# Performance work log

Measured on AMD Instinct MI355X. Metric: run time of the kernel, lower is better.

## Reference

```python
import jax, jax.numpy as jnp
import numpy as np

EPS = 1e-7  # K.epsilon()
ROUTINGS = 3

def squash(v, axis=-1):
    s2 = jnp.sum(jnp.square(v), axis=axis, keepdims=True)
    scale = s2 / (1.0 + s2)
    return scale * v / jnp.sqrt(s2 + EPS)

def setup_inputs() -> dict:
    key = jax.random.key(0)
    k1, k2 = jax.random.split(key)
    B, N, I, D, E = 16, 64, 2048, 32, 16
    x = jax.random.normal(k1, (B, I, E), dtype=jnp.float32)
    # glorot-uniform-ish scale for W [N, I, D, E]
    limit = np.sqrt(6.0 / (E + D)).astype(np.float32)
    W = jax.random.uniform(k2, (N, I, D, E), dtype=jnp.float32, minval=-limit, maxval=limit)
    return {"x": x, "W": W}

def reference(x, W):
    # x: [B, I, E]; W: [N, I, D, E]
    # u_hat[b,n,i,d] = sum_e W[n,i,d,e] * x[b,i,e]
    u_hat = jnp.einsum('nide,bie->bnid', W, x)  # [B, N, I, D]
    B, N, I, _ = u_hat.shape
    b = jnp.zeros((B, N, I), dtype=u_hat.dtype)
    outputs = None
    for i in range(ROUTINGS):
        c = jax.nn.softmax(b, axis=1)                     # softmax over num_capsule
        s = jnp.einsum('bni,bnid->bnd', c, u_hat)         # weighted sum
        outputs = squash(s)                               # [B, N, D]
        if i < ROUTINGS - 1:
            b = b + jnp.einsum('bnd,bnid->bni', outputs, u_hat)
    return outputs
```

## Files before the change

### kernel.cpp

```cpp
#include <hip/hip_runtime.h>
#include <cstdint>


#define B_ 16
#define N_ 64
#define I_ 2048
#define D_ 32
#define E_ 16
#define EPS_ 1e-7f
#define IPER_ 8
#define NCHUNK_ 256
#define GRIDP_ 512
#define SROW_ 2048
#define NOUT_ 32768
#define PSTRIDE_ 32768
#define WN4_ 262144

template <int CTRL>
__device__ __forceinline__ float dppf(float v) {
  return __int_as_float(
      __builtin_amdgcn_update_dpp(0, __float_as_int(v), CTRL, 0xF, 0xF, true));
}

__device__ __forceinline__ void chunk_u(const float4 wa0, const float4 wa1,
                                        const float* __restrict__ xr,
                                        int k, int q, float& u0, float& u1)
{
  float p0[4], p1[4];
#pragma unroll
  for (int j = 0; j < 4; ++j) {
    const float4 xv = *(const float4*)&xr[(4 * k + j) * E_ + 4 * q];
    p0[j] = wa0.x * xv.x + wa0.y * xv.y + wa0.z * xv.z + wa0.w * xv.w;
    p1[j] = wa1.x * xv.x + wa1.y * xv.y + wa1.z * xv.z + wa1.w * xv.w;
  }
  {
    const float r0 = p0[0] + dppf<0xB1>(p0[0]);
    const float r1 = p0[1] + dppf<0xB1>(p0[1]);
    const float r2 = p0[2] + dppf<0xB1>(p0[2]);
    const float r3 = p0[3] + dppf<0xB1>(p0[3]);
    const float sa = (q & 1) ? r1 : r0;
    const float sb = (q & 1) ? r3 : r2;
    const float a0 = sa + dppf<0x4E>(sa);
    const float a1 = sb + dppf<0x4E>(sb);
    u0 = (q & 2) ? a1 : a0;
  }
  {
    const float r0 = p1[0] + dppf<0xB1>(p1[0]);
    const float r1 = p1[1] + dppf<0xB1>(p1[1]);
    const float r2 = p1[2] + dppf<0xB1>(p1[2]);
    const float r3 = p1[3] + dppf<0xB1>(p1[3]);
    const float sa = (q & 1) ? r1 : r0;
    const float sb = (q & 1) ? r3 : r2;
    const float a0 = sa + dppf<0x4E>(sa);
    const float a1 = sb + dppf<0x4E>(sb);
    u1 = (q & 2) ? a1 : a0;
  }
}

template <int MODE>
__global__ __launch_bounds__(512)
__attribute__((amdgpu_waves_per_eu(4, 4)))
void caps_pass(
    const float* __restrict__ W,
    const float* __restrict__ x,
    const float* __restrict__ vtot,
    float* __restrict__ out,
    int use_part)
{
  const int t = threadIdx.x;
  const int w = t >> 6;
  const int l = t & 63;
  const int q = l & 3;
  const int dd = l >> 2;

  const int orig = blockIdx.x;
  const int h = (orig >> 3) & 1;
  const int ic = (orig & 7) | ((orig >> 4) << 3);
  const int i0 = ic * IPER_;

  __shared__ float x_lds[IPER_ * 8 * E_];
  __shared__ float2 u_st[16 * 512];
  __shared__ float l2[N_ * 33];
  __shared__ float c_lds[N_ * 9];

  for (int j = t; j < IPER_ * 8 * E_; j += 512) {
    const int ii = j >> 7, bl = (j >> 4) & 7, e = j & 15;
    x_lds[j] = x[((size_t)(h * 8 + bl) * I_ + (i0 + ii)) * E_ + e];
  }
  __syncthreads();

  float acc0[8][2], acc1[8][2];
#pragma unroll
  for (int nn = 0; nn < 8; ++nn)
#pragma unroll
    for (int k = 0; k < 2; ++k) { acc0[nn][k] = 0.f; acc1[nn][k] = 0.f; }

  float vt0[8][2], vt1[8][2];
  if (MODE == 1) {
#pragma unroll
    for (int nn = 0; nn < 8; ++nn)
#pragma unroll
      for (int k = 0; k < 2; ++k) {
        const size_t va = (size_t)(h * 8 + 4 * k + q) * SROW_ +
                          (size_t)(8 * w + nn) * D_ + dd;
        vt0[nn][k] = vtot[va];
        vt1[nn][k] = vtot[va + 16];
      }
  }

  const float4* Wbase = (const float4*)W + (((size_t)(8 * w) * I_ + i0) << 7);

#pragma unroll 1
  for (int ii = 0; ii < IPER_; ++ii) {
    const float* xr = &x_lds[ii * (8 * E_)];

#pragma unroll
    for (int g = 0; g < 4; ++g) {
      const float4* W0 = Wbase + (size_t)(2 * g) * WN4_ + ii * 128;
      const float4* W1 = W0 + WN4_;
      const float4 a0 = W0[l], a1 = W0[64 + l];
      const float4 b0 = W1[l], b1 = W1[64 + l];
#pragma unroll
      for (int s = 0; s < 2; ++s) {
        const int nn = 2 * g + s;
        const float4 wv0 = s ? b0 : a0;
        const float4 wv1 = s ? b1 : a1;
#pragma unroll
        for (int k = 0; k < 2; ++k) {
          float u0, u1;
          chunk_u(wv0, wv1, xr, k, q, u0, u1);
          if (MODE == 0) {
            acc0[nn][k] += u0;
            acc1[nn][k] += u1;
          } else {
            u_st[(nn * 2 + k) * 512 + t] = make_float2(u0, u1);
            float lp = vt0[nn][k] * u0 + vt1[nn][k] * u1;
            lp += dppf<0x124>(lp);
            lp += dppf<0x128>(lp);
            if ((l & 12) == 0)
              l2[(8 * w + nn) * 33 + (4 * k + q) * 4 + (l >> 4)] = lp;
          }
        }
      }
    }

    if (MODE == 1) {
      __syncthreads();
      {
        const int bw = t >> 6, j = t & 63;
        const int base = j * 33 + bw * 4;
        const float raw = l2[base] + l2[base + 1] + l2[base + 2] + l2[base + 3];
        float m = raw;
#pragma unroll
        for (int off = 32; off; off >>= 1) m = fmaxf(m, __shfl_xor(m, off));
        const float e = __expf(raw - m);
        float den = e;
#pragma unroll
        for (int off = 32; off; off >>= 1) den += __shfl_xor(den, off);
        c_lds[j * 9 + bw] = e / den;
      }
      __syncthreads();
#pragma unroll
      for (int nn = 0; nn < 8; ++nn)
#pragma unroll
        for (int k = 0; k < 2; ++k) {
          const float2 u = u_st[(nn * 2 + k) * 512 + t];
          const float cc = c_lds[(8 * w + nn) * 9 + 4 * k + q];
          acc0[nn][k] += cc * u.x;
          acc1[nn][k] += cc * u.y;
        }
    }
  }

  const float sc = (MODE == 0) ? (1.f / 64.f) : 1.f;
  float* base = out + (use_part ? (size_t)ic * PSTRIDE_ : 0);
#pragma unroll
  for (int nn = 0; nn < 8; ++nn) {
#pragma unroll
    for (int k = 0; k < 2; ++k) {
      const int b = h * 8 + 4 * k + q, n = 8 * w + nn;
      const size_t a = (size_t)b * SROW_ + (size_t)n * D_ + dd;
      if (use_part) {
        base[a] = acc0[nn][k] * sc;
        base[a + 16] = acc1[nn][k] * sc;
      } else {
        atomicAdd(&base[a], acc0[nn][k] * sc);
        atomicAdd(&base[a + 16], acc1[nn][k] * sc);
      }
    }
  }
}

template <int ACCMODE>
__global__ __launch_bounds__(256) void reduce_squash(
    const float* __restrict__ part, const float* __restrict__ s_single,
    float* __restrict__ dst, int use_part)
{
  const int g = blockIdx.x * 256 + threadIdx.x;
  float sum;
  if (use_part) {
    sum = 0.f;
#pragma unroll 8
    for (int p = 0; p < NCHUNK_; ++p) sum += part[(size_t)p * PSTRIDE_ + g];
  } else {
    sum = s_single[g];
  }
  float s2 = sum * sum;
#pragma unroll
  for (int off = 16; off; off >>= 1) s2 += __shfl_xor(s2, off);
  const float f = s2 / ((1.f + s2) * sqrtf(s2 + EPS_));
  if (ACCMODE == 0) dst[g] = sum * f;
  else dst[g] += sum * f;
}

extern "C" void kernel_launch(void* const* d_in, const int* in_sizes, int n_in,
                              void* d_out, int out_size, void* d_ws, size_t ws_size,
                              hipStream_t stream)
{
  const float* x = (const float*)d_in[0];
  const float* W = (const float*)d_in[1];
  float* s = (float*)d_out;
  float* vtot = (float*)d_ws;
  float* part = vtot + NOUT_;

  const size_t need =
      ((size_t)NOUT_ + (size_t)NCHUNK_ * PSTRIDE_) * sizeof(float);
  const int use_part = (ws_size >= need) ? 1 : 0;
  float* pass_out = use_part ? part : s;
  const size_t sbytes = (size_t)NOUT_ * sizeof(float);

  if (!use_part) hipMemsetAsync(s, 0, sbytes, stream);
  caps_pass<0><<<GRIDP_, 512, 0, stream>>>(W, x, vtot, pass_out, use_part);
  reduce_squash<0><<<128, 256, 0, stream>>>(part, s, vtot, use_part);

  if (!use_part) hipMemsetAsync(s, 0, sbytes, stream);
  caps_pass<1><<<GRIDP_, 512, 0, stream>>>(W, x, vtot, pass_out, use_part);
  reduce_squash<1><<<128, 256, 0, stream>>>(part, s, vtot, use_part);

  if (!use_part) hipMemsetAsync(s, 0, sbytes, stream);
  caps_pass<1><<<GRIDP_, 512, 0, stream>>>(W, x, vtot, pass_out, use_part);
  reduce_squash<0><<<128, 256, 0, stream>>>(part, s, s, use_part);
}
```

Before: 313.0 us.

## Split batch across four block groups to double grid and raise occupancy

Each block now handles 4 batch rows instead of 8, so the grid doubles to 1024 blocks. Per-thread accumulators, shared-memory buffers and the routing-softmax work shrink accordingly, and the waves-per-EU hint is relaxed to allow up to 8 waves. This targets latency hiding and occupancy in the pass kernels. The cost is that each W tile is now fetched by twice as many blocks, which increases global/L2 traffic for W, and half the threads sit idle during the softmax step.

```diff
diff --git a/kernel.cpp b/kernel.cpp
--- a/kernel.cpp
+++ b/kernel.cpp
@@ -7,10 +7,11 @@
 #define I_ 2048
 #define D_ 32
 #define E_ 16
+#define QB_ 4
 #define EPS_ 1e-7f
 #define IPER_ 8
 #define NCHUNK_ 256
-#define GRIDP_ 512
+#define GRIDP_ 1024
 #define SROW_ 2048
 #define NOUT_ 32768
 #define PSTRIDE_ 32768
@@ -22,14 +23,14 @@
       __builtin_amdgcn_update_dpp(0, __float_as_int(v), CTRL, 0xF, 0xF, true));
 }
 
-__device__ __forceinline__ void chunk_u(const float4 wa0, const float4 wa1,
-                                        const float* __restrict__ xr,
-                                        int k, int q, float& u0, float& u1)
+__device__ __forceinline__ void chunk4(const float4 wa0, const float4 wa1,
+                                       const float* __restrict__ xr,
+                                       int q, float& u0, float& u1)
 {
   float p0[4], p1[4];
 #pragma unroll
   for (int j = 0; j < 4; ++j) {
-    const float4 xv = *(const float4*)&xr[(4 * k + j) * E_ + 4 * q];
+    const float4 xv = *(const float4*)&xr[j * E_ + 4 * q];
     p0[j] = wa0.x * xv.x + wa0.y * xv.y + wa0.z * xv.z + wa0.w * xv.w;
     p1[j] = wa1.x * xv.x + wa1.y * xv.y + wa1.z * xv.z + wa1.w * xv.w;
   }
@@ -59,7 +60,7 @@
 
 template <int MODE>
 __global__ __launch_bounds__(512)
-__attribute__((amdgpu_waves_per_eu(4, 4)))
+__attribute__((amdgpu_waves_per_eu(8)))
 void caps_pass(
     const float* __restrict__ W,
     const float* __restrict__ x,
@@ -74,45 +75,41 @@
   const int dd = l >> 2;
 
   const int orig = blockIdx.x;
-  const int h = (orig >> 3) & 1;
-  const int ic = (orig & 7) | ((orig >> 4) << 3);
+  const int h = (orig >> 3) & 3;
+  const int ic = (orig & 7) | ((orig >> 5) << 3);
   const int i0 = ic * IPER_;
 
-  __shared__ float x_lds[IPER_ * 8 * E_];
-  __shared__ float2 u_st[16 * 512];
-  __shared__ float l2[N_ * 33];
-  __shared__ float c_lds[N_ * 9];
-
-  for (int j = t; j < IPER_ * 8 * E_; j += 512) {
-    const int ii = j >> 7, bl = (j >> 4) & 7, e = j & 15;
-    x_lds[j] = x[((size_t)(h * 8 + bl) * I_ + (i0 + ii)) * E_ + e];
+  __shared__ float x_lds[IPER_ * QB_ * E_];
+  __shared__ float2 u_st[(MODE == 1) ? 8 * 512 : 1];
+  __shared__ float l2[(MODE == 1) ? N_ * 17 : 1];
+  __shared__ float c_lds[(MODE == 1) ? N_ * 5 : 1];
+
+  {
+    const int ii = t >> 6, bl = (t >> 4) & 3, e = t & 15;
+    x_lds[t] = x[((size_t)(h * QB_ + bl) * I_ + (i0 + ii)) * E_ + e];
   }
   __syncthreads();
 
-  float acc0[8][2], acc1[8][2];
-#pragma unroll
-  for (int nn = 0; nn < 8; ++nn)
-#pragma unroll
-    for (int k = 0; k < 2; ++k) { acc0[nn][k] = 0.f; acc1[nn][k] = 0.f; }
-
-  float vt0[8][2], vt1[8][2];
+  float acc0[8], acc1[8];
+#pragma unroll
+  for (int nn = 0; nn < 8; ++nn) { acc0[nn] = 0.f; acc1[nn] = 0.f; }
+
+  float vt0[8], vt1[8];
   if (MODE == 1) {
 #pragma unroll
-    for (int nn = 0; nn < 8; ++nn)
-#pragma unroll
-      for (int k = 0; k < 2; ++k) {
-        const size_t va = (size_t)(h * 8 + 4 * k + q) * SROW_ +
-                          (size_t)(8 * w + nn) * D_ + dd;
-        vt0[nn][k] = vtot[va];
-        vt1[nn][k] = vtot[va + 16];
-      }
+    for (int nn = 0; nn < 8; ++nn) {
+      const size_t va = (size_t)(h * QB_ + q) * SROW_ +
+                        (size_t)(8 * w + nn) * D_ + dd;
+      vt0[nn] = vtot[va];
+      vt1[nn] = vtot[va + 16];
+    }
   }
 
   const float4* Wbase = (const float4*)W + (((size_t)(8 * w) * I_ + i0) << 7);
 
 #pragma unroll 1
   for (int ii = 0; ii < IPER_; ++ii) {
-    const float* xr = &x_lds[ii * (8 * E_)];
+    const float* xr = &x_lds[ii * (QB_ * E_)];
 
 #pragma unroll
     for (int g = 0; g < 4; ++g) {
@@ -123,23 +120,18 @@
 #pragma unroll
       for (int s = 0; s < 2; ++s) {
         const int nn = 2 * g + s;
-        const float4 wv0 = s ? b0 : a0;
-        const float4 wv1 = s ? b1 : a1;
-#pragma unroll
-        for (int k = 0; k < 2; ++k) {
-          float u0, u1;
-          chunk_u(wv0, wv1, xr, k, q, u0, u1);
-          if (MODE == 0) {
-            acc0[nn][k] += u0;
-            acc1[nn][k] += u1;
-          } else {
-            u_st[(nn * 2 + k) * 512 + t] = make_float2(u0, u1);
-            float lp = vt0[nn][k] * u0 + vt1[nn][k] * u1;
-            lp += dppf<0x124>(lp);
-            lp += dppf<0x128>(lp);
-            if ((l & 12) == 0)
-              l2[(8 * w + nn) * 33 + (4 * k + q) * 4 + (l >> 4)] = lp;
-          }
+        float u0, u1;
+        chunk4(s ? b0 : a0, s ? b1 : a1, xr, q, u0, u1);
+        if (MODE == 0) {
+          acc0[nn] += u0;
+          acc1[nn] += u1;
+        } else {
+          u_st[nn * 512 + t] = make_float2(u0, u1);
+          float lp = vt0[nn] * u0 + vt1[nn] * u1;
+          lp += dppf<0x124>(lp);
+          lp += dppf<0x128>(lp);
+          if ((l & 12) == 0)
+            l2[(8 * w + nn) * 17 + q * 4 + (l >> 4)] = lp;
         }
       }
     }
@@ -148,27 +140,28 @@
       __syncthreads();
       {
         const int bw = t >> 6, j = t & 63;
-        const int base = j * 33 + bw * 4;
-        const float raw = l2[base] + l2[base + 1] + l2[base + 2] + l2[base + 3];
-        float m = raw;
-#pragma unroll
-        for (int off = 32; off; off >>= 1) m = fmaxf(m, __shfl_xor(m, off));
-        const float e = __expf(raw - m);
-        float den = e;
-#pragma unroll
-        for (int off = 32; off; off >>= 1) den += __shfl_xor(den, off);
-        c_lds[j * 9 + bw] = e / den;
+        if (bw < QB_) {
+          const int base = j * 17 + bw * 4;
+          const float raw =
+              l2[base] + l2[base + 1] + l2[base + 2] + l2[base + 3];
+          float m = raw;
+#pragma unroll
+          for (int off = 32; off; off >>= 1) m = fmaxf(m, __shfl_xor(m, off));
+          const float e = __expf(raw - m);
+          float den = e;
+#pragma unroll
+          for (int off = 32; off; off >>= 1) den += __shfl_xor(den, off);
+          c_lds[j * 5 + bw] = e / den;
+        }
       }
       __syncthreads();
 #pragma unroll
-      for (int nn = 0; nn < 8; ++nn)
-#pragma unroll
-        for (int k = 0; k < 2; ++k) {
-          const float2 u = u_st[(nn * 2 + k) * 512 + t];
-          const float cc = c_lds[(8 * w + nn) * 9 + 4 * k + q];
-          acc0[nn][k] += cc * u.x;
-          acc1[nn][k] += cc * u.y;
-        }
+      for (int nn = 0; nn < 8; ++nn) {
+        const float2 u = u_st[nn * 512 + t];
+        const float cc = c_lds[(8 * w + nn) * 5 + q];
+        acc0[nn] += cc * u.x;
+        acc1[nn] += cc * u.y;
+      }
     }
   }
 
@@ -176,17 +169,14 @@
   float* base = out + (use_part ? (size_t)ic * PSTRIDE_ : 0);
 #pragma unroll
   for (int nn = 0; nn < 8; ++nn) {
-#pragma unroll
-    for (int k = 0; k < 2; ++k) {
-      const int b = h * 8 + 4 * k + q, n = 8 * w + nn;
-      const size_t a = (size_t)b * SROW_ + (size_t)n * D_ + dd;
-      if (use_part) {
-        base[a] = acc0[nn][k] * sc;
-        base[a + 16] = acc1[nn][k] * sc;
-      } else {
-        atomicAdd(&base[a], acc0[nn][k] * sc);
-        atomicAdd(&base[a + 16], acc1[nn][k] * sc);
-      }
+    const int b = h * QB_ + q, n = 8 * w + nn;
+    const size_t a = (size_t)b * SROW_ + (size_t)n * D_ + dd;
+    if (use_part) {
+      base[a] = acc0[nn] * sc;
+      base[a + 16] = acc1[nn] * sc;
+    } else {
+      atomicAdd(&base[a], acc0[nn] * sc);
+      atomicAdd(&base[a + 16], acc1[nn] * sc);
     }
   }
 }
```

Result: slower. 1.130 ms (+260.9%).
